# Optimization experiments

Hardware: AMD Instinct MI355X
Metric: run time of the kernel (lower is better)

The kernel has to match this reference:

```python
import jax, jax.numpy as jnp
import numpy as np

B, N, U, D, E = 4, 20000, 64, 1, 640000
F = U + D  # node feature dim fed to TransformerConv (state || inputs)
SCALE = 1.0 / float(np.sqrt(U))
NEG = -1e30


def setup_inputs() -> dict:
    key = jax.random.key(0)
    ks = jax.random.split(key, 20)

    def glorot(k, shape):
        s = float(np.sqrt(2.0 / (shape[0] + shape[1])))
        return jax.random.normal(k, shape, jnp.float32) * s

    inp = {
        'inputs': jax.random.normal(ks[0], (B, N), jnp.float32),
        'state': jax.random.normal(ks[1], (B, N * U), jnp.float32),
        'edge_src': jax.random.randint(ks[2], (E,), 0, N),
        'edge_dst': jax.random.randint(ks[3], (E,), 0, N),
        # TransformerConv(U+D -> U, heads=1, concat=False): query/key/value/skip linears
        'Wq': glorot(ks[4], (F, U)), 'bq': jnp.zeros((U,), jnp.float32),
        'Wk': glorot(ks[5], (F, U)), 'bk': jnp.zeros((U,), jnp.float32),
        'Wv': glorot(ks[6], (F, U)), 'bv': jnp.zeros((U,), jnp.float32),
        'Ws': glorot(ks[7], (F, U)), 'bs': jnp.zeros((U,), jnp.float32),
        # GRULinear 1: (U + D) -> 2U ; GRULinear 2: (U + D) -> U
        'W1': glorot(ks[8], (U + D, 2 * U)), 'b1': jnp.zeros((2 * U,), jnp.float32),
        'W2': glorot(ks[9], (U + D, U)), 'b2': jnp.zeros((U,), jnp.float32),
    }
    return inp


def _transformer_conv_masked(x, src, dst, Wq, bq, Wk, bk, Wv, bv, Ws, bs):
    """x: (B, N, F). PyG TransformerConv heads=1 concat=False with node/edge
    masking as in remove_nodes_and_edges (keep nodes with x[:, -7] != 0)."""
    node_mask = x[..., -7] != 0  # (B, N)
    emask = (node_mask[:, src] & node_mask[:, dst]).astype(x.dtype)  # (B, E)

    q = x @ Wq + bq  # (B, N, U)
    k = x @ Wk + bk
    v = x @ Wv + bv

    scores = jnp.einsum('beu,beu->be', q[:, dst], k[:, src]) * SCALE  # (B, E)
    scores_m = jnp.where(emask > 0, scores, NEG)
    m = jnp.full((x.shape[0], N), NEG, x.dtype).at[:, dst].max(scores_m)  # (B, N)
    e = jnp.exp(jnp.where(emask > 0, scores - m[:, dst], 0.0)) * emask  # (B, E)

    denom = jnp.zeros((x.shape[0], N), x.dtype).at[:, dst].add(e)  # (B, N)
    num = jnp.zeros((x.shape[0], N, U), x.dtype).at[:, dst].add(e[..., None] * v[:, src])
    agg = jnp.where(denom[..., None] > 0, num / jnp.maximum(denom, 1e-16)[..., None], 0.0)

    out = agg + (x @ Ws + bs)  # root/skip connection
    # nodes that were filtered out keep their original first-U feature columns (= old state)
    return jnp.where(node_mask[..., None], out, x[..., :U])  # (B, N, U)


def reference(inputs, state, edge_src, edge_dst, Wq, bq, Wk, bk, Wv, bv, Ws, bs,
              W1, b1, W2, b2):
    xin = inputs.reshape(B, N, D)
    h = state.reshape(B, N, U)
    # _gc3: TransformerConv over [state || inputs]
    x = jnp.concatenate([h, xin], axis=-1)  # (B, N, F)
    h2 = _transformer_conv_masked(x, edge_src, edge_dst, Wq, bq, Wk, bk, Wv, bv, Ws, bs)
    # GRU gates
    cat1 = jnp.concatenate([xin, h2], axis=-1)  # (B, N, U+D)
    value = jax.nn.sigmoid(cat1 @ W1 + b1)  # (B, N, 2U)
    reset, z = value[..., :U], value[..., U:]
    c = jnp.tanh(jnp.concatenate([xin, reset * h2], axis=-1) @ W2 + b2)
    new_state = (1.0 - z) * h2 + z * c
    return new_state.reshape(B, N * U)
```

## Files before the change

kernel.cpp:

```cpp
#include <hip/hip_runtime.h>
#include <hip/hip_bf16.h>

#define BB 4
#define NN 20000
#define UU 64
#define EE 640000
#define FF 65
#define SCALE_F 0.125f
#define PREP_BLOCKS 2500
#define SCAT_BLOCKS 2500

typedef unsigned short u16;
typedef unsigned long long u64;

static inline size_t align_up(size_t x) { return (x + 255) & ~(size_t)255; }

__device__ __forceinline__ float u2f(unsigned int u) { return __uint_as_float(u); }
__device__ __forceinline__ u16 f2bf(float f) {
    __hip_bfloat16 h = __float2bfloat16(f);
    return *reinterpret_cast<u16*>(&h);
}

__global__ __launch_bounds__(256) void prep_scatter_kernel(
    const float* __restrict__ state, const float* __restrict__ inputs,
    const float* __restrict__ Wk, const float* __restrict__ bk,
    const float* __restrict__ Wv, const float* __restrict__ bv,
    u16* __restrict__ kbuf, u16* __restrict__ vbuf,
    unsigned char* __restrict__ maskb,
    const int* __restrict__ edst, const int* __restrict__ esrc,
    int* __restrict__ counts, u16* __restrict__ bins, int cap) {
    int role = blockIdx.x & 1;
    int sub  = blockIdx.x >> 1;
    if (role) {
        int e = sub * 256 + threadIdx.x;
        if (e < EE) {
            int d = edst[e], s = esrc[e];
            if ((unsigned)d < (unsigned)NN && (unsigned)s < (unsigned)NN) {
                int pos = atomicAdd(&counts[d], 1);
                if (pos < cap) bins[d * cap + pos] = (u16)s;
            }
        }
        return;
    }
    int w = threadIdx.x >> 6, lane = threadIdx.x & 63;
    int gb = (sub * 4 + w) * 8;
    __shared__ float xs[4][8][66];
#pragma unroll
    for (int j = 0; j < 8; ++j) {
        int g = gb + j;
        xs[w][j][lane] = state[(size_t)g * UU + lane];
        if (lane == 0) xs[w][j][64] = inputs[g];
    }
    __syncthreads();

    float ak[8], av[8];
#pragma unroll
    for (int j = 0; j < 8; ++j) { ak[j] = 0.f; av[j] = 0.f; }
    for (int f = 0; f < FF; ++f) {
        float wk = Wk[f * UU + lane], wv = Wv[f * UU + lane];
#pragma unroll
        for (int j = 0; j < 8; ++j) {
            float xv = xs[w][j][f];
            ak[j] += xv * wk; av[j] += xv * wv;
        }
    }
    float bkl = bk[lane], bvl = bv[lane];
#pragma unroll
    for (int j = 0; j < 8; ++j) {
        int g = gb + j;
        kbuf[(size_t)g * UU + lane] = f2bf(ak[j] + bkl);
        vbuf[(size_t)g * UU + lane] = f2bf(av[j] + bvl);
        if (lane == 0) maskb[g] = (xs[w][j][58] != 0.0f) ? 1 : 0;
    }
}

__global__ __launch_bounds__(256) void fused_fast(
    const float* __restrict__ state, const float* __restrict__ inputs,
    const float* __restrict__ Wq, const float* __restrict__ bq,
    const float* __restrict__ Ws, const float* __restrict__ bs,
    const float* __restrict__ W1, const float* __restrict__ b1,
    const float* __restrict__ W2, const float* __restrict__ b2,
    const u16* __restrict__ kbuf, const u16* __restrict__ vbuf,
    const unsigned char* __restrict__ maskb,
    const int* __restrict__ counts, const u16* __restrict__ bins, int cap,
    float* __restrict__ out) {
    int w = threadIdx.x >> 6, lane = threadIdx.x & 63;
    int hl = lane & 31, hf = lane >> 5;

    int bid = blockIdx.x;
    int xcd = bid & 7;
    int b   = xcd >> 1;
    int ib  = ((bid >> 3) << 1) | (xcd & 1);
    int gb  = b * NN + ib * 16 + w * 4;

    __shared__ float xs[4][4][66];
    __shared__ float qs[4][4][68];
    __shared__ u64   pl[4][64];

#pragma unroll
    for (int j = 0; j < 4; ++j) {
        int g = gb + j;
        xs[w][j][lane] = state[(size_t)g * UU + lane];
        if (lane == 0) xs[w][j][64] = inputs[g];
    }
    __syncthreads();

    float aq[4], as_[4];
#pragma unroll
    for (int j = 0; j < 4; ++j) { aq[j] = 0.f; as_[j] = 0.f; }
    for (int f = 0; f < FF; ++f) {
        float wq = Wq[f * UU + lane], ws = Ws[f * UU + lane];
#pragma unroll
        for (int j = 0; j < 4; ++j) {
            float xv = xs[w][j][f];
            aq[j] += xv * wq; as_[j] += xv * ws;
        }
    }
    float bql = bq[lane], bsl = bs[lane];
#pragma unroll
    for (int j = 0; j < 4; ++j) {
        aq[j] = (aq[j] + bql) * SCALE_F;
        as_[j] += bsl;
        qs[w][j][lane] = aq[j];
    }
    __syncthreads();

    bool mg[4];
#pragma unroll
    for (int j = 0; j < 4; ++j) mg[j] = (xs[w][j][58] != 0.0f);

    const unsigned char* mb = maskb + (size_t)b * NN;
    const u16* kb = kbuf + (size_t)b * NN * UU;
    const u16* vb = vbuf + (size_t)b * NN * UU;
    int nb = gb - b * NN;

    int cum[5]; cum[0] = 0;
    int ebase[4];
#pragma unroll
    for (int j = 0; j < 4; ++j) {
        int dg = counts[nb + j];
        dg = min(max(dg, 0), cap);
        if (!mg[j]) dg = 0;
        cum[j + 1] = cum[j] + dg;
        ebase[j] = (nb + j) * cap - cum[j];
    }
    int total = cum[4];

    float acE[4], acO[4], l[4];
#pragma unroll
    for (int j = 0; j < 4; ++j) { acE[j] = 0.f; acO[j] = 0.f; l[j] = 0.f; }

    const unsigned* vbw = (const unsigned*)vb;

#pragma unroll 1
    for (int tbase = 0; tbase < total; tbase += 64) {
        int i = tbase + lane;
        float p = 0.f; int srow = 0;
        if (i < total) {
            int jl = (i >= cum[1]) + (i >= cum[2]) + (i >= cum[3]);
            int s = bins[ebase[jl] + i];
            if (mb[s]) {
                srow = s;
                const uint4* kp = (const uint4*)(kb + ((size_t)s << 6));
                const float* qrow = &qs[w][0][0] + jl * 68;
                float d0 = 0.f, d1 = 0.f, d2 = 0.f, d3 = 0.f;
#pragma unroll
                for (int c = 0; c < 8; ++c) {
                    uint4 kk = kp[c];
                    const float4 qa = *(const float4*)&qrow[c * 8];
                    const float4 qc = *(const float4*)&qrow[c * 8 + 4];
                    d0 += u2f(kk.x << 16) * qa.x; d1 += u2f(kk.x & 0xFFFF0000u) * qa.y;
                    d2 += u2f(kk.y << 16) * qa.z; d3 += u2f(kk.y & 0xFFFF0000u) * qa.w;
                    d0 += u2f(kk.z << 16) * qc.x; d1 += u2f(kk.z & 0xFFFF0000u) * qc.y;
                    d2 += u2f(kk.w << 16) * qc.z; d3 += u2f(kk.w & 0xFFFF0000u) * qc.w;
                }
                float sc = (d0 + d1) + (d2 + d3);
                p = __expf(sc);
            }
        }
        pl[w][lane] = ((u64)(unsigned)srow << 32) | (u64)__float_as_uint(p);
        __builtin_amdgcn_wave_barrier();

#pragma unroll
        for (int j = 0; j < 4; ++j) {
            int lo = max(cum[j], tbase);
            int hi = min(cum[j + 1], tbase + 64);
#pragma unroll 1
            for (int s0 = lo; s0 < hi; s0 += 8) {
#pragma unroll
                for (int k2 = 0; k2 < 4; ++k2) {
                    int ss = s0 + 2 * k2 + hf;
                    int sidx = min(ss, hi - 1) - tbase;
                    u64 pk = pl[w][sidx];
                    float pj = (ss < hi) ? u2f((unsigned)pk) : 0.f;
                    unsigned sj = (unsigned)(pk >> 32);
                    unsigned v2 = vbw[(sj << 5) | (unsigned)hl];
                    acE[j] += pj * u2f(v2 << 16);
                    acO[j] += pj * u2f(v2 & 0xFFFF0000u);
                    l[j]   += pj;
                }
            }
        }
        __builtin_amdgcn_wave_barrier();
    }

#pragma unroll
    for (int j = 0; j < 4; ++j) {
        float lj = l[j]   + __shfl_xor(l[j],   32, 64);
        float aE = acE[j] + __shfl_xor(acE[j], 32, 64);
        float aO = acO[j] + __shfl_xor(acO[j], 32, 64);
        float vE = __shfl(aE, lane >> 1, 64);
        float vO = __shfl(aO, lane >> 1, 64);
        float acc = (lane & 1) ? vO : vE;
        float agg = (lj > 0.f) ? acc / fmaxf(lj, 1e-16f) : 0.f;
        float h2 = mg[j] ? (agg + as_[j]) : xs[w][j][lane];
        xs[w][j][lane] = h2;
    }
    __syncthreads();

    float xin[4];
#pragma unroll
    for (int j = 0; j < 4; ++j) xin[j] = xs[w][j][64];
    float a1[4], a2[4];
#pragma unroll
    for (int j = 0; j < 4; ++j) { a1[j] = xin[j] * W1[lane]; a2[j] = xin[j] * W1[UU + lane]; }
    for (int f = 0; f < UU; ++f) {
        float w1a = W1[(f + 1) * 128 + lane], w1b = W1[(f + 1) * 128 + UU + lane];
#pragma unroll
        for (int j = 0; j < 4; ++j) {
            float hv = xs[w][j][f];
            a1[j] += hv * w1a; a2[j] += hv * w1b;
        }
    }
    float b1a = b1[lane], b1b = b1[UU + lane];
    float rst[4], z[4];
#pragma unroll
    for (int j = 0; j < 4; ++j) {
        rst[j] = 1.f / (1.f + __expf(-(a1[j] + b1a)));
        z[j]   = 1.f / (1.f + __expf(-(a2[j] + b1b)));
        qs[w][j][lane] = rst[j] * xs[w][j][lane];
    }
    __syncthreads();

    float a3[4];
#pragma unroll
    for (int j = 0; j < 4; ++j) a3[j] = xin[j] * W2[lane];
    for (int f = 0; f < UU; ++f) {
        float w2v = W2[(f + 1) * UU + lane];
#pragma unroll
        for (int j = 0; j < 4; ++j) a3[j] += qs[w][j][f] * w2v;
    }
    float b2l = b2[lane];
#pragma unroll
    for (int j = 0; j < 4; ++j) {
        float a = a3[j] + b2l;
        float aa = fabsf(a), tt = __expf(-2.f * aa);
        float c = copysignf((1.f - tt) / (1.f + tt), a);
        float h2v = xs[w][j][lane];
        out[(size_t)(gb + j) * UU + lane] = (1.f - z[j]) * h2v + z[j] * c;
    }
}

extern "C" void kernel_launch(void* const* d_in, const int* in_sizes, int n_in,
                              void* d_out, int out_size, void* d_ws, size_t ws_size,
                              hipStream_t stream) {
    const float* inputs = (const float*)d_in[0];
    const float* state  = (const float*)d_in[1];
    if (in_sizes[0] != BB * NN) { inputs = (const float*)d_in[1]; state = (const float*)d_in[0]; }
    const int*   esrc   = (const int*)d_in[2];
    const int*   edst   = (const int*)d_in[3];
    const float* Wq = (const float*)d_in[4];
    const float* bq = (const float*)d_in[5];
    const float* Wk = (const float*)d_in[6];
    const float* bk = (const float*)d_in[7];
    const float* Wv = (const float*)d_in[8];
    const float* bv = (const float*)d_in[9];
    const float* Ws = (const float*)d_in[10];
    const float* bs = (const float*)d_in[11];
    const float* W1 = (const float*)d_in[12];
    const float* b1 = (const float*)d_in[13];
    const float* W2 = (const float*)d_in[14];
    const float* b2 = (const float*)d_in[15];
    float* out = (float*)d_out;

    char* base = (char*)d_ws;
    size_t ofs = 0;
    int* counts = (int*)(base + ofs); ofs = align_up(ofs + (size_t)NN * 4);
    unsigned char* maskb = (unsigned char*)(base + ofs); ofs = align_up(ofs + (size_t)BB * NN);
    u16* kbuf = (u16*)(base + ofs); ofs = align_up(ofs + (size_t)BB * NN * UU * 2);
    u16* vbuf = (u16*)(base + ofs); ofs = align_up(ofs + (size_t)BB * NN * UU * 2);
    u16* bins = (u16*)(base + ofs);
    size_t avail = (ws_size > ofs) ? (ws_size - ofs) : 0;
    int cap = (int)(avail / ((size_t)NN * 2));
    if (cap > 128) cap = 128;
    if (cap < 64)  cap = 64;
    (void)n_in; (void)out_size;

    hipMemsetAsync(counts, 0, (size_t)NN * 4, stream);
    prep_scatter_kernel<<<PREP_BLOCKS + SCAT_BLOCKS, 256, 0, stream>>>(
        state, inputs, Wk, bk, Wv, bv, kbuf, vbuf, maskb,
        edst, esrc, counts, bins, cap);
    fused_fast<<<(BB * NN) / 16, 256, 0, stream>>>(state, inputs, Wq, bq,
                                                   Ws, bs, W1, b1, W2, b2,
                                                   kbuf, vbuf, maskb,
                                                   counts, bins, cap, out);
}
```

Measured before the change: 333.4 us.

## Gather V rows as 8-byte loads over quarter-wave splits and drop block barriers

The value aggregation loop now has each quarter-wave handle one edge, with 16 lanes each loading a uint2 (4 bf16 values), so 4 edges are processed per step instead of 2 half-wave edges with 4-byte loads. The final cross-lane reduction uses xor shuffles plus an LDS scratch transpose. Block-wide __syncthreads are replaced with wave barriers because each wave only touches its own shared-memory rows. Inner FMA loops get unroll-by-4 pragmas and the LDS rows are padded to 68 floats with 16-byte alignment. The aim is fewer gather instructions and less synchronization, at the cost of more registers and extra shuffle/LDS steps in the epilogue.

```diff
diff --git a/kernel.cpp b/kernel.cpp
--- a/kernel.cpp
+++ b/kernel.cpp
@@ -20,6 +20,7 @@
     __hip_bfloat16 h = __float2bfloat16(f);
     return *reinterpret_cast<u16*>(&h);
 }
+__device__ __forceinline__ void wbar() { __builtin_amdgcn_wave_barrier(); }
 
 __global__ __launch_bounds__(256) void prep_scatter_kernel(
     const float* __restrict__ state, const float* __restrict__ inputs,
@@ -44,18 +45,19 @@
     }
     int w = threadIdx.x >> 6, lane = threadIdx.x & 63;
     int gb = (sub * 4 + w) * 8;
-    __shared__ float xs[4][8][66];
+    __shared__ __align__(16) float xs[4][8][68];
 #pragma unroll
     for (int j = 0; j < 8; ++j) {
         int g = gb + j;
         xs[w][j][lane] = state[(size_t)g * UU + lane];
         if (lane == 0) xs[w][j][64] = inputs[g];
     }
-    __syncthreads();
+    wbar();
 
     float ak[8], av[8];
 #pragma unroll
     for (int j = 0; j < 8; ++j) { ak[j] = 0.f; av[j] = 0.f; }
+#pragma unroll 4
     for (int f = 0; f < FF; ++f) {
         float wk = Wk[f * UU + lane], wv = Wv[f * UU + lane];
 #pragma unroll
@@ -85,7 +87,7 @@
     const int* __restrict__ counts, const u16* __restrict__ bins, int cap,
     float* __restrict__ out) {
     int w = threadIdx.x >> 6, lane = threadIdx.x & 63;
-    int hl = lane & 31, hf = lane >> 5;
+    int qq = lane >> 4, c16 = lane & 15;
 
     int bid = blockIdx.x;
     int xcd = bid & 7;
@@ -93,9 +95,10 @@
     int ib  = ((bid >> 3) << 1) | (xcd & 1);
     int gb  = b * NN + ib * 16 + w * 4;
 
-    __shared__ float xs[4][4][66];
-    __shared__ float qs[4][4][68];
-    __shared__ u64   pl[4][64];
+    __shared__ __align__(16) float xs[4][4][68];
+    __shared__ __align__(16) float qs[4][4][68];
+    __shared__ __align__(16) u64   pl[4][64];
+    __shared__ __align__(16) float rs[4][4][68];
 
 #pragma unroll
     for (int j = 0; j < 4; ++j) {
@@ -103,11 +106,12 @@
         xs[w][j][lane] = state[(size_t)g * UU + lane];
         if (lane == 0) xs[w][j][64] = inputs[g];
     }
-    __syncthreads();
+    wbar();
 
     float aq[4], as_[4];
 #pragma unroll
     for (int j = 0; j < 4; ++j) { aq[j] = 0.f; as_[j] = 0.f; }
+#pragma unroll 4
     for (int f = 0; f < FF; ++f) {
         float wq = Wq[f * UU + lane], ws = Ws[f * UU + lane];
 #pragma unroll
@@ -119,11 +123,10 @@
     float bql = bq[lane], bsl = bs[lane];
 #pragma unroll
     for (int j = 0; j < 4; ++j) {
-        aq[j] = (aq[j] + bql) * SCALE_F;
         as_[j] += bsl;
-        qs[w][j][lane] = aq[j];
-    }
-    __syncthreads();
+        qs[w][j][lane] = (aq[j] + bql) * SCALE_F;
+    }
+    wbar();
 
     bool mg[4];
 #pragma unroll
@@ -146,11 +149,14 @@
     }
     int total = cum[4];
 
-    float acE[4], acO[4], l[4];
-#pragma unroll
-    for (int j = 0; j < 4; ++j) { acE[j] = 0.f; acO[j] = 0.f; l[j] = 0.f; }
-
-    const unsigned* vbw = (const unsigned*)vb;
+    float ac[4][4], l[4];
+#pragma unroll
+    for (int j = 0; j < 4; ++j) {
+        ac[j][0] = 0.f; ac[j][1] = 0.f; ac[j][2] = 0.f; ac[j][3] = 0.f;
+        l[j] = 0.f;
+    }
+
+    const uint2* vb2 = (const uint2*)vb;
 
 #pragma unroll 1
     for (int tbase = 0; tbase < total; tbase += 64) {
@@ -179,85 +185,93 @@
             }
         }
         pl[w][lane] = ((u64)(unsigned)srow << 32) | (u64)__float_as_uint(p);
-        __builtin_amdgcn_wave_barrier();
+        wbar();
 
 #pragma unroll
         for (int j = 0; j < 4; ++j) {
             int lo = max(cum[j], tbase);
             int hi = min(cum[j + 1], tbase + 64);
 #pragma unroll 1
-            for (int s0 = lo; s0 < hi; s0 += 8) {
-#pragma unroll
-                for (int k2 = 0; k2 < 4; ++k2) {
-                    int ss = s0 + 2 * k2 + hf;
-                    int sidx = min(ss, hi - 1) - tbase;
-                    u64 pk = pl[w][sidx];
-                    float pj = (ss < hi) ? u2f((unsigned)pk) : 0.f;
-                    unsigned sj = (unsigned)(pk >> 32);
-                    unsigned v2 = vbw[(sj << 5) | (unsigned)hl];
-                    acE[j] += pj * u2f(v2 << 16);
-                    acO[j] += pj * u2f(v2 & 0xFFFF0000u);
-                    l[j]   += pj;
-                }
+            for (int ss0 = (lo & ~3); ss0 < hi; ss0 += 4) {
+                int ss = ss0 + qq;
+                bool val = (ss >= lo) & (ss < hi);
+                int sidx = (val ? ss : lo) - tbase;
+                u64 pk = pl[w][sidx];
+                float pj = val ? u2f((unsigned)pk) : 0.f;
+                unsigned sj = (unsigned)(pk >> 32);
+                uint2 v2 = vb2[(sj << 4) | (unsigned)c16];
+                ac[j][0] += pj * u2f(v2.x << 16);
+                ac[j][1] += pj * u2f(v2.x & 0xFFFF0000u);
+                ac[j][2] += pj * u2f(v2.y << 16);
+                ac[j][3] += pj * u2f(v2.y & 0xFFFF0000u);
+                l[j] += pj;
             }
         }
-        __builtin_amdgcn_wave_barrier();
-    }
-
-#pragma unroll
-    for (int j = 0; j < 4; ++j) {
-        float lj = l[j]   + __shfl_xor(l[j],   32, 64);
-        float aE = acE[j] + __shfl_xor(acE[j], 32, 64);
-        float aO = acO[j] + __shfl_xor(acO[j], 32, 64);
-        float vE = __shfl(aE, lane >> 1, 64);
-        float vO = __shfl(aO, lane >> 1, 64);
-        float acc = (lane & 1) ? vO : vE;
+        wbar();
+    }
+
+    float* scr = (float*)&pl[w][0];
+#pragma unroll
+    for (int j = 0; j < 4; ++j) {
+        float lj = l[j];
+        float a0 = ac[j][0], a1 = ac[j][1], a2 = ac[j][2], a3 = ac[j][3];
+        lj += __shfl_xor(lj, 16, 64); lj += __shfl_xor(lj, 32, 64);
+        a0 += __shfl_xor(a0, 16, 64); a0 += __shfl_xor(a0, 32, 64);
+        a1 += __shfl_xor(a1, 16, 64); a1 += __shfl_xor(a1, 32, 64);
+        a2 += __shfl_xor(a2, 16, 64); a2 += __shfl_xor(a2, 32, 64);
+        a3 += __shfl_xor(a3, 16, 64); a3 += __shfl_xor(a3, 32, 64);
+        if (qq == 0) *(float4*)&scr[c16 * 4] = make_float4(a0, a1, a2, a3);
+        wbar();
+        float acc = scr[lane];
         float agg = (lj > 0.f) ? acc / fmaxf(lj, 1e-16f) : 0.f;
         float h2 = mg[j] ? (agg + as_[j]) : xs[w][j][lane];
+        wbar();
         xs[w][j][lane] = h2;
     }
-    __syncthreads();
+    wbar();
 
     float xin[4];
 #pragma unroll
     for (int j = 0; j < 4; ++j) xin[j] = xs[w][j][64];
-    float a1[4], a2[4];
-#pragma unroll
-    for (int j = 0; j < 4; ++j) { a1[j] = xin[j] * W1[lane]; a2[j] = xin[j] * W1[UU + lane]; }
+    float a1v[4], a2v[4];
+#pragma unroll
+    for (int j = 0; j < 4; ++j) { a1v[j] = xin[j] * W1[lane]; a2v[j] = xin[j] * W1[UU + lane]; }
+#pragma unroll 4
     for (int f = 0; f < UU; ++f) {
         float w1a = W1[(f + 1) * 128 + lane], w1b = W1[(f + 1) * 128 + UU + lane];
 #pragma unroll
         for (int j = 0; j < 4; ++j) {
             float hv = xs[w][j][f];
-            a1[j] += hv * w1a; a2[j] += hv * w1b;
+            a1v[j] += hv * w1a; a2v[j] += hv * w1b;
         }
     }
     float b1a = b1[lane], b1b = b1[UU + lane];
     float rst[4], z[4];
 #pragma unroll
     for (int j = 0; j < 4; ++j) {
-        rst[j] = 1.f / (1.f + __expf(-(a1[j] + b1a)));
-        z[j]   = 1.f / (1.f + __expf(-(a2[j] + b1b)));
-        qs[w][j][lane] = rst[j] * xs[w][j][lane];
-    }
-    __syncthreads();
-
-    float a3[4];
-#pragma unroll
-    for (int j = 0; j < 4; ++j) a3[j] = xin[j] * W2[lane];
+        rst[j] = 1.f / (1.f + __expf(-(a1v[j] + b1a)));
+        z[j]   = 1.f / (1.f + __expf(-(a2v[j] + b1b)));
+        rs[w][j][lane] = rst[j] * xs[w][j][lane];
+    }
+    wbar();
+
+    float a3v[4];
+#pragma unroll
+    for (int j = 0; j < 4; ++j) a3v[j] = xin[j] * W2[lane];
+#pragma unroll 4
     for (int f = 0; f < UU; ++f) {
         float w2v = W2[(f + 1) * UU + lane];
 #pragma unroll
-        for (int j = 0; j < 4; ++j) a3[j] += qs[w][j][f] * w2v;
+        for (int j = 0; j < 4; ++j) a3v[j] += rs[w][j][f] * w2v;
     }
     float b2l = b2[lane];
 #pragma unroll
     for (int j = 0; j < 4; ++j) {
-        float a = a3[j] + b2l;
+        float a = a3v[j] + b2l;
         float aa = fabsf(a), tt = __expf(-2.f * aa);
         float c = copysignf((1.f - tt) / (1.f + tt), a);
-        float h2v = xs[w][j][lane];
-        out[(size_t)(gb + j) * UU + lane] = (1.f - z[j]) * h2v + z[j] * c;
+        float h2v_ = xs[w][j][lane];
+        out[(size_t)(gb + j) * UU + lane] = (1.f - z[j]) * h2v_ + z[j] * c;
     }
 }
 
```

Result: slower. 395.4 us (+18.6%).
